# Kernel optimization log

Hardware: AMD Instinct MI355X
Metric: run time of the kernel (lower is better)

Reference implementation:

```python
import jax, jax.numpy as jnp
import numpy as np

N = 100000       # nodes
E = 1600000      # edges (before self loops)
D = 128          # emb_dim
L = 5            # num_layer
NBOND = 62       # num_bond_type
NNODE = 2159     # num_node_type + 2
BN_EPS = 1e-5


def setup_inputs() -> dict:
    key = jax.random.key(0)
    ks = jax.random.split(key, 8)
    x = jax.random.randint(ks[0], (N, 1), 0, NNODE)
    edge_index = jax.random.randint(ks[1], (2, E), 0, N)
    edge_attr = jax.random.randint(ks[2], (E, 1), 0, NBOND)
    x_emb = jax.random.normal(ks[3], (NNODE, D), dtype=jnp.float32) * 0.02
    lin_w = jax.random.normal(ks[4], (L, D, D), dtype=jnp.float32) * (1.0 / np.sqrt(D))
    lin_b = jnp.zeros((L, D), jnp.float32)
    edge_tab = jax.random.normal(ks[5], (L, NBOND, D), dtype=jnp.float32) * 0.02
    bn_gamma = jnp.ones((L, D), jnp.float32)
    bn_beta = jnp.zeros((L, D), jnp.float32)
    return {"x": x, "edge_index": edge_index, "edge_attr": edge_attr,
            "x_emb": x_emb, "lin_w": lin_w, "lin_b": lin_b,
            "edge_tab": edge_tab, "bn_gamma": bn_gamma, "bn_beta": bn_beta}


def reference(x, edge_index, edge_attr, x_emb, lin_w, lin_b, edge_tab, bn_gamma, bn_beta):
    # node embedding lookup: x_embedding(x[:, 0])
    h = x_emb[x[:, 0]]                                  # [N, D]

    # add self loops (same for every layer in the torch code)
    loop = jnp.arange(N)
    src = jnp.concatenate([edge_index[0], loop])        # [E+N] = j (source)
    dst = jnp.concatenate([edge_index[1], loop])        # [E+N] = i (target)
    eids = jnp.concatenate([edge_attr[:, 0], jnp.zeros((N,), edge_attr.dtype)])

    # GCN symmetric norm: deg from row (=src), deg_inv_sqrt[row]*deg_inv_sqrt[col]
    deg = jax.ops.segment_sum(jnp.ones(src.shape, h.dtype), src, num_segments=N)
    dinv = jnp.where(deg > 0, jax.lax.rsqrt(deg), jnp.zeros_like(deg))
    norm = (dinv[src] * dinv[dst])[:, None]             # [E+N, 1]

    for l in range(L):
        # linear transform of nodes
        hl = h @ lin_w[l].T + lin_b[l]                  # [N, D]
        # message: norm * (x_j + edge_embedding), gather from source nodes
        msg = norm * (hl[src] + edge_tab[l][eids])      # [E+N, D]
        # aggr='add': scatter_add into target nodes
        agg = jax.ops.segment_sum(msg, dst, num_segments=N)  # [N, D]
        # BatchNorm1d (training-mode batch statistics, biased variance)
        mean = agg.mean(axis=0)
        var = jnp.mean((agg - mean) ** 2, axis=0)
        h = (agg - mean) * jax.lax.rsqrt(var + BN_EPS) * bn_gamma[l] + bn_beta[l]
        if l < L - 1:
            h = jax.nn.relu(h)
        # dropout with drop_ratio=0 is identity
    # JK == 'last'
    return h
```

## Files before the change

kernel.cpp:

```cpp
#include <hip/hip_runtime.h>

#define NN 100000
#define NE 1600000
#define NT (NE + NN)
#define DD 128
#define NL 5
#define NB 62
#define BN_EPS 1e-5f
#define NBUCK 391
#define PSUMNB 6250
#define RED1 128

typedef unsigned short ushort_t;
typedef unsigned int uint_t;
typedef short bf8 __attribute__((ext_vector_type(8)));
typedef float f32x4 __attribute__((ext_vector_type(4)));

static __device__ __forceinline__ float4 ld4(const float* p) { return *(const float4*)p; }

static __device__ __forceinline__ float bfhi(uint_t u) {
    uint_t x = u & 0xFFFF0000u;
    return __builtin_bit_cast(float, x);
}
static __device__ __forceinline__ float bflo(uint_t u) {
    uint_t x = u << 16;
    return __builtin_bit_cast(float, x);
}
static __device__ __forceinline__ ushort_t f2bf(float f) {
    uint_t u = __builtin_bit_cast(uint_t, f);
    u += 0x7FFFu + ((u >> 16) & 1u);
    return (ushort_t)(u >> 16);
}

static __device__ __forceinline__ void accum8(float* acc, uint4 hv, uint4 ev, float nr) {
    acc[0] = fmaf(nr, bflo(hv.x) + bflo(ev.x), acc[0]);
    acc[1] = fmaf(nr, bfhi(hv.x) + bfhi(ev.x), acc[1]);
    acc[2] = fmaf(nr, bflo(hv.y) + bflo(ev.y), acc[2]);
    acc[3] = fmaf(nr, bfhi(hv.y) + bfhi(ev.y), acc[3]);
    acc[4] = fmaf(nr, bflo(hv.z) + bflo(ev.z), acc[4]);
    acc[5] = fmaf(nr, bfhi(hv.z) + bfhi(ev.z), acc[5]);
    acc[6] = fmaf(nr, bflo(hv.w) + bflo(ev.w), acc[6]);
    acc[7] = fmaf(nr, bfhi(hv.w) + bfhi(ev.w), acc[7]);
}


__global__ void k_init(int* gbh_d, int* gbh_s, float* scale, float* shift,
                       int* row_ptr) {
    int i = blockIdx.x * 256 + threadIdx.x;
    if (i < NBUCK) { gbh_d[i] = 0; gbh_s[i] = 0; }
    if (i < DD) { scale[i] = 1.f; shift[i] = 0.f; }
    if (i == 0) row_ptr[NN] = NT;
}

__global__ void k_cvt(const float* __restrict__ src, ushort_t* __restrict__ dst,
                      int total) {
    int i = blockIdx.x * 256 + threadIdx.x;
    if (i < total) dst[i] = f2bf(src[i]);
}

__global__ __launch_bounds__(256) void k_binhist(const int* __restrict__ ei,
                                                 int* __restrict__ gbh_d,
                                                 int* __restrict__ gbh_s) {
    __shared__ int hd[NBUCK], hs[NBUCK];
    int tid = threadIdx.x;
    for (int b = tid; b < NBUCK; b += 256) { hd[b] = 0; hs[b] = 0; }
    __syncthreads();
    for (int idx = blockIdx.x * 256 + tid; idx < NT; idx += gridDim.x * 256) {
        int d = (idx < NE) ? ei[NE + idx] : idx - NE;
        atomicAdd(&hd[d >> 8], 1);
        if (idx < NE) atomicAdd(&hs[ei[idx] >> 8], 1);
    }
    __syncthreads();
    for (int b = tid; b < NBUCK; b += 256) {
        if (hd[b]) atomicAdd(&gbh_d[b], hd[b]);
        if (hs[b]) atomicAdd(&gbh_s[b], hs[b]);
    }
}

__global__ void k_scan391(const int* __restrict__ gbh_d, const int* __restrict__ gbh_s,
                          int* __restrict__ bb_d, int* __restrict__ cur_d,
                          int* __restrict__ bb_s, int* __restrict__ cur_s) {
    __shared__ int s[512];
    const int* g = blockIdx.x ? gbh_s : gbh_d;
    int* bb = blockIdx.x ? bb_s : bb_d;
    int* cur = blockIdx.x ? cur_s : cur_d;
    int t = threadIdx.x;
    int v = (t < NBUCK) ? g[t] : 0;
    s[t] = v;
    __syncthreads();
    for (int off = 1; off < 512; off <<= 1) {
        int val = (t >= off) ? s[t - off] : 0;
        __syncthreads();
        s[t] += val;
        __syncthreads();
    }
    if (t < NBUCK) { int e = s[t] - v; bb[t] = e; cur[t] = e; }
    if (t == 511) bb[NBUCK] = s[511];
}

#define CHUNK 4096
__global__ __launch_bounds__(256) void k_scat2(const int* __restrict__ ei,
                                               const int* __restrict__ ea,
                                               int* __restrict__ cur_d,
                                               int* __restrict__ cur_s,
                                               uint_t* __restrict__ rec_d,
                                               int* __restrict__ rec_s) {
    __shared__ int lhd[NBUCK], lbd[NBUCK], lhs[NBUCK], lbs[NBUCK];
    int tid = threadIdx.x;
    for (int b = tid; b < NBUCK; b += 256) { lhd[b] = 0; lhs[b] = 0; }
    __syncthreads();
    int base = blockIdx.x * CHUNK;
    uint_t rd[16];
    int rs[16], bkd[16], bks[16];
#pragma unroll
    for (int k = 0; k < 16; ++k) {
        int idx = base + tid + k * 256;
        bkd[k] = -1; bks[k] = -1;
        if (idx < NT) {
            int s, d, eid;
            if (idx < NE) {
                s = ei[idx]; d = ei[NE + idx]; eid = ea[idx];
                bks[k] = s >> 8; rs[k] = s;
                atomicAdd(&lhs[bks[k]], 1);
            } else {
                s = d = idx - NE; eid = 0;
            }
            bkd[k] = d >> 8;
            rd[k] = (uint_t)s | ((uint_t)eid << 17) | ((uint_t)(d & 255) << 24);
            atomicAdd(&lhd[bkd[k]], 1);
        }
    }
    __syncthreads();
    for (int b = tid; b < NBUCK; b += 256) {
        if (lhd[b]) lbd[b] = atomicAdd(&cur_d[b], lhd[b]);
        if (lhs[b]) lbs[b] = atomicAdd(&cur_s[b], lhs[b]);
    }
    __syncthreads();
    for (int b = tid; b < NBUCK; b += 256) { lhd[b] = 0; lhs[b] = 0; }
    __syncthreads();
#pragma unroll
    for (int k = 0; k < 16; ++k) {
        if (bkd[k] >= 0) {
            int rk = atomicAdd(&lhd[bkd[k]], 1);
            rec_d[lbd[bkd[k]] + rk] = rd[k];
        }
        if (bks[k] >= 0) {
            int rk = atomicAdd(&lhs[bks[k]], 1);
            rec_s[lbs[bks[k]] + rk] = rs[k];
        }
    }
}

__global__ __launch_bounds__(256) void k_srcfin(const int* __restrict__ rec,
                                                const int* __restrict__ bb,
                                                float* __restrict__ dinv) {
    __shared__ int h[256];
    int tid = threadIdx.x;
    h[tid] = 0;
    __syncthreads();
    int lo = bb[blockIdx.x], hi = bb[blockIdx.x + 1];
    for (int i = lo + tid; i < hi; i += 256) atomicAdd(&h[rec[i] & 255], 1);
    __syncthreads();
    int v = blockIdx.x * 256 + tid;
    if (v < NN) dinv[v] = rsqrtf((float)(h[tid] + 1));
}

__global__ __launch_bounds__(256) void k_dstfin(const uint_t* __restrict__ rec,
                                                const int* __restrict__ bb,
                                                const float* __restrict__ dinv,
                                                int* __restrict__ row_ptr,
                                                int* __restrict__ s_pack,
                                                float* __restrict__ s_norm) {
    __shared__ int h[256], sc[256], rpE[256];
    int tid = threadIdx.x;
    h[tid] = 0;
    __syncthreads();
    int lo = bb[blockIdx.x], hi = bb[blockIdx.x + 1];
    for (int i = lo + tid; i < hi; i += 256) atomicAdd(&h[(rec[i] >> 24) & 255], 1);
    __syncthreads();
    sc[tid] = h[tid];
    __syncthreads();
    for (int off = 1; off < 256; off <<= 1) {
        int val = (tid >= off) ? sc[tid - off] : 0;
        __syncthreads();
        sc[tid] += val;
        __syncthreads();
    }
    rpE[tid] = sc[tid] - h[tid];
    int v = blockIdx.x * 256 + tid;
    if (v < NN) row_ptr[v] = lo + rpE[tid];
    h[tid] = 0;
    __syncthreads();
    for (int i = lo + tid; i < hi; i += 256) {
        uint_t u = rec[i];
        int dl = (u >> 24) & 255;
        int rk = atomicAdd(&h[dl], 1);
        int slot = lo + rpE[dl] + rk;
        int s = u & 0x1FFFF;
        int e = (u >> 17) & 0x3F;
        s_pack[slot] = s | (e << 20);
        s_norm[slot] = dinv[s] * dinv[(blockIdx.x << 8) + dl];
    }
}

__global__ void k_h0b(const int* __restrict__ x, const float* __restrict__ emb,
                      ushort_t* __restrict__ Xb, int n) {
    int v = blockIdx.x * 16 + (threadIdx.x >> 4);
    if (v >= n) return;
    int c8 = (threadIdx.x & 15) * 8;
    const float* src = &emb[x[v] * DD + c8];
    uint_t pk[4];
#pragma unroll
    for (int j = 0; j < 4; ++j)
        pk[j] = (uint_t)f2bf(src[2 * j]) | ((uint_t)f2bf(src[2 * j + 1]) << 16);
    *(uint4*)&Xb[(size_t)v * DD + c8] = make_uint4(pk[0], pk[1], pk[2], pk[3]);
}


__global__ __launch_bounds__(256, 2) void k_gemm(const ushort_t* __restrict__ Xb,
                                                 const ushort_t* __restrict__ Wb,
                                                 const float* __restrict__ bias,
                                                 const float* __restrict__ scale,
                                                 const float* __restrict__ shift,
                                                 ushort_t* __restrict__ C,
                                                 int n, int relu) {
    __shared__ ushort_t As[128 * DD];
    __shared__ ushort_t Bs[128 * DD];
    const int tid = threadIdx.x;
    const int r0 = blockIdx.x * 128;
    const int rl = tid >> 4;
    const int kg = tid & 15;

    float sc[8], sh[8];
    *(float4*)&sc[0] = ld4(&scale[kg * 8]);
    *(float4*)&sc[4] = ld4(&scale[kg * 8 + 4]);
    *(float4*)&sh[0] = ld4(&shift[kg * 8]);
    *(float4*)&sh[4] = ld4(&shift[kg * 8 + 4]);

#pragma unroll
    for (int it = 0; it < 8; ++it) {
        int row = rl + it * 16;
        int grow = r0 + row;
        uint4 v = make_uint4(0, 0, 0, 0);
        if (grow < n) v = *(const uint4*)&Xb[(size_t)grow * DD + kg * 8];
        uint_t pk[4];
        const uint_t* pv = (const uint_t*)&v;
#pragma unroll
        for (int j = 0; j < 4; ++j) {
            float lo = fmaf(bflo(pv[j]), sc[2 * j], sh[2 * j]);
            float hi = fmaf(bfhi(pv[j]), sc[2 * j + 1], sh[2 * j + 1]);
            if (relu) { lo = fmaxf(lo, 0.f); hi = fmaxf(hi, 0.f); }
            pk[j] = (uint_t)f2bf(lo) | ((uint_t)f2bf(hi) << 16);
        }
        *(uint4*)&As[row * DD + (kg ^ (row & 7)) * 8] = make_uint4(pk[0], pk[1], pk[2], pk[3]);
        uint4 wv = *(const uint4*)&Wb[row * DD + kg * 8];
        *(uint4*)&Bs[row * DD + (kg ^ (row & 7)) * 8] = wv;
    }
    __syncthreads();

    const int w = tid >> 6;
    const int lane = tid & 63;
    const int lr = lane & 15;
    const int lg = lane >> 4;

    f32x4 acc[2][8];
#pragma unroll
    for (int rf = 0; rf < 2; ++rf)
#pragma unroll
        for (int cf = 0; cf < 8; ++cf)
#pragma unroll
            for (int r = 0; r < 4; ++r) acc[rf][cf][r] = 0.f;

#pragma unroll
    for (int ks = 0; ks < 4; ++ks) {
        int kgg = ks * 4 + lg;
        bf8 a0, a1;
        {
            int row = w * 32 + lr;
            a0 = *(bf8*)&As[row * DD + (kgg ^ (row & 7)) * 8];
            row += 16;
            a1 = *(bf8*)&As[row * DD + (kgg ^ (row & 7)) * 8];
        }
#pragma unroll
        for (int cf = 0; cf < 8; ++cf) {
            int col = cf * 16 + lr;
            bf8 b = *(bf8*)&Bs[col * DD + (kgg ^ (col & 7)) * 8];
            acc[0][cf] = __builtin_amdgcn_mfma_f32_16x16x32_bf16(a0, b, acc[0][cf], 0, 0, 0);
            acc[1][cf] = __builtin_amdgcn_mfma_f32_16x16x32_bf16(a1, b, acc[1][cf], 0, 0, 0);
        }
    }

#pragma unroll
    for (int cf = 0; cf < 8; ++cf) {
        int col = cf * 16 + lr;
        float bi = bias[col];
#pragma unroll
        for (int rf = 0; rf < 2; ++rf) {
#pragma unroll
            for (int r = 0; r < 4; ++r) {
                int grow = r0 + w * 32 + rf * 16 + lg * 4 + r;
                if (grow < n) C[(size_t)grow * DD + col] = f2bf(acc[rf][cf][r] + bi);
            }
        }
    }
}

__global__ __launch_bounds__(256) void k_agg(const ushort_t* __restrict__ hl,
                                             const ushort_t* __restrict__ etab,
                                             const int* __restrict__ row_ptr,
                                             const int* __restrict__ s_pack,
                                             const float* __restrict__ s_norm,
                                             ushort_t* __restrict__ aggb,
                                             float* __restrict__ psumA,
                                             float* __restrict__ psumB, int n) {
    __shared__ float lsA[4][DD], lsB[4][DD];
    int tid = threadIdx.x;

    int v = blockIdx.x * 16 + (tid >> 4);
    int lane8 = (tid & 15) * 8;
    int p0 = row_ptr[v], p1 = row_ptr[v + 1];
    float acc[8];
#pragma unroll
    for (int j = 0; j < 8; ++j) acc[j] = 0.f;

    int p = p0;
    for (; p + 4 <= p1; p += 4) {
        int c0 = s_pack[p], c1 = s_pack[p + 1], c2 = s_pack[p + 2], c3 = s_pack[p + 3];
        float n0 = s_norm[p], n1 = s_norm[p + 1], n2 = s_norm[p + 2], n3 = s_norm[p + 3];
        uint4 h0 = *(const uint4*)&hl[(size_t)(c0 & 0xFFFFF) * DD + lane8];
        uint4 h1 = *(const uint4*)&hl[(size_t)(c1 & 0xFFFFF) * DD + lane8];
        uint4 h2 = *(const uint4*)&hl[(size_t)(c2 & 0xFFFFF) * DD + lane8];
        uint4 h3 = *(const uint4*)&hl[(size_t)(c3 & 0xFFFFF) * DD + lane8];
        uint4 e0 = *(const uint4*)&etab[(c0 >> 20) * DD + lane8];
        uint4 e1 = *(const uint4*)&etab[(c1 >> 20) * DD + lane8];
        uint4 e2 = *(const uint4*)&etab[(c2 >> 20) * DD + lane8];
        uint4 e3 = *(const uint4*)&etab[(c3 >> 20) * DD + lane8];
        accum8(acc, h0, e0, n0);
        accum8(acc, h1, e1, n1);
        accum8(acc, h2, e2, n2);
        accum8(acc, h3, e3, n3);
    }
    for (; p < p1; ++p) {
        int c = s_pack[p];
        float nr = s_norm[p];
        uint4 hv = *(const uint4*)&hl[(size_t)(c & 0xFFFFF) * DD + lane8];
        uint4 ev = *(const uint4*)&etab[(c >> 20) * DD + lane8];
        accum8(acc, hv, ev, nr);
    }

    uint_t pk[4];
#pragma unroll
    for (int j = 0; j < 4; ++j)
        pk[j] = (uint_t)f2bf(acc[2 * j]) | ((uint_t)f2bf(acc[2 * j + 1]) << 16);
    *(uint4*)&aggb[(size_t)v * DD + lane8] = make_uint4(pk[0], pk[1], pk[2], pk[3]);

    float s0[8], s1[8];
#pragma unroll
    for (int j = 0; j < 8; ++j) { s0[j] = acc[j]; s1[j] = acc[j] * acc[j]; }
#pragma unroll
    for (int m = 16; m <= 32; m <<= 1) {
#pragma unroll
        for (int j = 0; j < 8; ++j) {
            s0[j] += __shfl_xor(s0[j], m);
            s1[j] += __shfl_xor(s1[j], m);
        }
    }
    int wv = tid >> 6;
    int lane = tid & 63;
    if (lane < 16) {
#pragma unroll
        for (int j = 0; j < 8; ++j) {
            lsA[wv][lane8 + j] = s0[j];
            lsB[wv][lane8 + j] = s1[j];
        }
    }
    __syncthreads();
    if (tid < DD) {
        psumA[(size_t)blockIdx.x * DD + tid] =
            lsA[0][tid] + lsA[1][tid] + lsA[2][tid] + lsA[3][tid];
        psumB[(size_t)blockIdx.x * DD + tid] =
            lsB[0][tid] + lsB[1][tid] + lsB[2][tid] + lsB[3][tid];
    }
}

__global__ __launch_bounds__(256) void k_bnred(const float* __restrict__ psumA,
                                               const float* __restrict__ psumB,
                                               float* __restrict__ partA,
                                               float* __restrict__ partB) {
    __shared__ float sa[2][DD], sb[2][DD];
    int d = threadIdx.x & 127;
    int half = threadIdx.x >> 7;
    float a = 0.f, b = 0.f;
    int iend = min(blockIdx.x * 49 + 49, PSUMNB);
    for (int i = blockIdx.x * 49 + half; i < iend; i += 2) {
        a += psumA[(size_t)i * DD + d];
        b += psumB[(size_t)i * DD + d];
    }
    sa[half][d] = a; sb[half][d] = b;
    __syncthreads();
    if (threadIdx.x < DD) {
        partA[blockIdx.x * DD + d] = sa[0][d] + sa[1][d];
        partB[blockIdx.x * DD + d] = sb[0][d] + sb[1][d];
    }
}

__global__ __launch_bounds__(256) void k_bnfin(const float* __restrict__ partA,
                                               const float* __restrict__ partB,
                                               const float* __restrict__ gamma,
                                               const float* __restrict__ beta,
                                               float* __restrict__ scale,
                                               float* __restrict__ shift, int n) {
    __shared__ float sa[2][DD], sb[2][DD];
    int d = threadIdx.x & 127;
    int half = threadIdx.x >> 7;
    float a = 0.f, b = 0.f;
    for (int i = half; i < RED1; i += 2) {
        a += partA[i * DD + d];
        b += partB[i * DD + d];
    }
    sa[half][d] = a; sb[half][d] = b;
    __syncthreads();
    if (threadIdx.x < DD) {
        float s = sa[0][d] + sa[1][d];
        float ss = sb[0][d] + sb[1][d];
        float mean = s / (float)n;
        float var = ss / (float)n - mean * mean;
        float sc = gamma[d] * rsqrtf(var + BN_EPS);
        scale[d] = sc;
        shift[d] = beta[d] - mean * sc;
    }
}

__global__ void k_bnapply(const ushort_t* __restrict__ Xb, float* __restrict__ out,
                          const float* __restrict__ scale,
                          const float* __restrict__ shift, int total8) {
    int i = blockIdx.x * blockDim.x + threadIdx.x;
    int stride = gridDim.x * blockDim.x;
    for (; i < total8; i += stride) {
        int c8 = (i & 15) * 8;
        uint4 v = *(const uint4*)&Xb[(size_t)i * 8];
        float4 sc0 = ld4(&scale[c8]), sc1 = ld4(&scale[c8 + 4]);
        float4 sh0 = ld4(&shift[c8]), sh1 = ld4(&shift[c8 + 4]);
        float4 o0, o1;
        o0.x = fmaf(bflo(v.x), sc0.x, sh0.x);
        o0.y = fmaf(bfhi(v.x), sc0.y, sh0.y);
        o0.z = fmaf(bflo(v.y), sc0.z, sh0.z);
        o0.w = fmaf(bfhi(v.y), sc0.w, sh0.w);
        o1.x = fmaf(bflo(v.z), sc1.x, sh1.x);
        o1.y = fmaf(bfhi(v.z), sc1.y, sh1.y);
        o1.z = fmaf(bflo(v.w), sc1.z, sh1.z);
        o1.w = fmaf(bfhi(v.w), sc1.w, sh1.w);
        *(float4*)&out[(size_t)i * 8] = o0;
        *(float4*)&out[(size_t)i * 8 + 4] = o1;
    }
}


extern "C" void kernel_launch(void* const* d_in, const int* in_sizes, int n_in,
                              void* d_out, int out_size, void* d_ws, size_t ws_size,
                              hipStream_t stream) {
    const int* x        = (const int*)d_in[0];
    const int* ei       = (const int*)d_in[1];
    const int* ea       = (const int*)d_in[2];
    const float* x_emb  = (const float*)d_in[3];
    const float* lin_w  = (const float*)d_in[4];
    const float* lin_b  = (const float*)d_in[5];
    const float* etab   = (const float*)d_in[6];
    const float* gamma  = (const float*)d_in[7];
    const float* beta   = (const float*)d_in[8];
    float* OUT = (float*)d_out;

    char* w = (char*)d_ws;
    size_t off = 0;
    auto alloc = [&](size_t bytes) -> void* {
        off = (off + 255) & ~(size_t)255;
        void* p = w + off;
        off += bytes;
        return p;
    };
    ushort_t* Xb     = (ushort_t*)alloc((size_t)NN * DD * 2);
    ushort_t* hl     = (ushort_t*)alloc((size_t)NN * DD * 2);
    ushort_t* etabb  = (ushort_t*)alloc((size_t)NL * NB * DD * 2);
    ushort_t* Wb     = (ushort_t*)alloc((size_t)NL * DD * DD * 2);
    uint_t* rec_d    = (uint_t*)alloc((size_t)NT * 4);
    int*    rec_s    = (int*)alloc((size_t)NE * 4);
    int*   s_pack    = (int*)alloc((size_t)NT * 4);
    float* s_norm    = (float*)alloc((size_t)NT * 4);
    int*   rowp      = (int*)alloc((size_t)(NN + 1) * 4);
    float* dinv      = (float*)alloc((size_t)NN * 4);
    int*   gbh_d     = (int*)alloc((size_t)NBUCK * 4);
    int*   gbh_s     = (int*)alloc((size_t)NBUCK * 4);
    int*   bb_d      = (int*)alloc((size_t)(NBUCK + 1) * 4);
    int*   bb_s      = (int*)alloc((size_t)(NBUCK + 1) * 4);
    int*   cur_d     = (int*)alloc((size_t)NBUCK * 4);
    int*   cur_s     = (int*)alloc((size_t)NBUCK * 4);
    float* psumA     = (float*)alloc((size_t)DD * PSUMNB * 4);
    float* psumB     = (float*)alloc((size_t)DD * PSUMNB * 4);
    float* partA     = (float*)alloc((size_t)DD * RED1 * 4);
    float* partB     = (float*)alloc((size_t)DD * RED1 * 4);
    float* scale     = (float*)alloc((size_t)DD * 4);
    float* shift     = (float*)alloc((size_t)DD * 4);

    const int etabTot = NL * NB * DD;
    const int wTot = NL * DD * DD;

    k_init<<<(NN + 255) / 256, 256, 0, stream>>>(gbh_d, gbh_s, scale, shift, rowp);
    k_cvt<<<(etabTot + 255) / 256, 256, 0, stream>>>(etab, etabb, etabTot);
    k_cvt<<<(wTot + 255) / 256, 256, 0, stream>>>(lin_w, Wb, wTot);
    k_binhist<<<256, 256, 0, stream>>>(ei, gbh_d, gbh_s);
    k_scan391<<<2, 512, 0, stream>>>(gbh_d, gbh_s, bb_d, cur_d, bb_s, cur_s);
    k_scat2<<<(NT + CHUNK - 1) / CHUNK, 256, 0, stream>>>(ei, ea, cur_d, cur_s,
                                                          rec_d, rec_s);
    k_srcfin<<<NBUCK, 256, 0, stream>>>(rec_s, bb_s, dinv);
    k_dstfin<<<NBUCK, 256, 0, stream>>>(rec_d, bb_d, dinv, rowp, s_pack, s_norm);
    k_h0b<<<(NN + 15) / 16, 256, 0, stream>>>(x, x_emb, Xb, NN);

    for (int l = 0; l < NL; ++l) {
        k_gemm<<<(NN + 127) / 128, 256, 0, stream>>>(Xb, Wb + (size_t)l * DD * DD,
                                                     lin_b + (size_t)l * DD,
                                                     scale, shift, hl, NN, l > 0 ? 1 : 0);
        k_agg<<<PSUMNB, 256, 0, stream>>>(hl, etabb + (size_t)l * NB * DD,
                                          rowp, s_pack, s_norm, Xb, psumA, psumB, NN);
        k_bnred<<<RED1, 256, 0, stream>>>(psumA, psumB, partA, partB);
        k_bnfin<<<1, 256, 0, stream>>>(partA, partB, gamma + (size_t)l * DD,
                                       beta + (size_t)l * DD, scale, shift, NN);
    }
    k_bnapply<<<(NN * DD / 8 + 255) / 256, 256, 0, stream>>>(Xb, OUT, scale, shift,
                                                             NN * DD / 8);
}
```

Before: 733.3 us.

## Split GEMM K into two halves with register prefetch; unroll gather by eight

The GEMM now stages K in two 64-wide halves and uses half the shared memory. The second half's global loads are issued before the first half's MFMAs so their latency overlaps compute, and launch_bounds no longer pins two blocks per CU. The aggregation kernel gains an 8-edge unrolled loop that issues more independent gathers before accumulating, raising memory-level parallelism. The cost is higher register pressure, which may lower occupancy, plus an extra barrier in the GEMM.

```diff
diff --git a/kernel.cpp b/kernel.cpp
--- a/kernel.cpp
+++ b/kernel.cpp
@@ -217,52 +217,66 @@
 }
 
 
-__global__ __launch_bounds__(256, 2) void k_gemm(const ushort_t* __restrict__ Xb,
-                                                 const ushort_t* __restrict__ Wb,
-                                                 const float* __restrict__ bias,
-                                                 const float* __restrict__ scale,
-                                                 const float* __restrict__ shift,
-                                                 ushort_t* __restrict__ C,
-                                                 int n, int relu) {
-    __shared__ ushort_t As[128 * DD];
-    __shared__ ushort_t Bs[128 * DD];
+__global__ __launch_bounds__(256) void k_gemm(const ushort_t* __restrict__ Xb,
+                                              const ushort_t* __restrict__ Wb,
+                                              const float* __restrict__ bias,
+                                              const float* __restrict__ scale,
+                                              const float* __restrict__ shift,
+                                              ushort_t* __restrict__ C,
+                                              int n, int relu) {
+    __shared__ ushort_t As[128 * 64];
+    __shared__ ushort_t Bs[128 * 64];
     const int tid = threadIdx.x;
     const int r0 = blockIdx.x * 128;
-    const int rl = tid >> 4;
-    const int kg = tid & 15;
-
-    float sc[8], sh[8];
-    *(float4*)&sc[0] = ld4(&scale[kg * 8]);
-    *(float4*)&sc[4] = ld4(&scale[kg * 8 + 4]);
-    *(float4*)&sh[0] = ld4(&shift[kg * 8]);
-    *(float4*)&sh[4] = ld4(&shift[kg * 8 + 4]);
-
-#pragma unroll
-    for (int it = 0; it < 8; ++it) {
-        int row = rl + it * 16;
-        int grow = r0 + row;
-        uint4 v = make_uint4(0, 0, 0, 0);
-        if (grow < n) v = *(const uint4*)&Xb[(size_t)grow * DD + kg * 8];
-        uint_t pk[4];
-        const uint_t* pv = (const uint_t*)&v;
-#pragma unroll
-        for (int j = 0; j < 4; ++j) {
-            float lo = fmaf(bflo(pv[j]), sc[2 * j], sh[2 * j]);
-            float hi = fmaf(bfhi(pv[j]), sc[2 * j + 1], sh[2 * j + 1]);
-            if (relu) { lo = fmaxf(lo, 0.f); hi = fmaxf(hi, 0.f); }
-            pk[j] = (uint_t)f2bf(lo) | ((uint_t)f2bf(hi) << 16);
-        }
-        *(uint4*)&As[row * DD + (kg ^ (row & 7)) * 8] = make_uint4(pk[0], pk[1], pk[2], pk[3]);
-        uint4 wv = *(const uint4*)&Wb[row * DD + kg * 8];
-        *(uint4*)&Bs[row * DD + (kg ^ (row & 7)) * 8] = wv;
-    }
-    __syncthreads();
+    const int skg = tid & 7;
+    const int srow = tid >> 3;
 
     const int w = tid >> 6;
     const int lane = tid & 63;
     const int lr = lane & 15;
     const int lg = lane >> 4;
 
+    float sc0[8], sh0[8], sc1[8], sh1[8];
+    *(float4*)&sc0[0] = ld4(&scale[skg * 8]);     *(float4*)&sc0[4] = ld4(&scale[skg * 8 + 4]);
+    *(float4*)&sh0[0] = ld4(&shift[skg * 8]);     *(float4*)&sh0[4] = ld4(&shift[skg * 8 + 4]);
+    *(float4*)&sc1[0] = ld4(&scale[64 + skg * 8]); *(float4*)&sc1[4] = ld4(&scale[64 + skg * 8 + 4]);
+    *(float4*)&sh1[0] = ld4(&shift[64 + skg * 8]); *(float4*)&sh1[4] = ld4(&shift[64 + skg * 8 + 4]);
+
+    uint4 ar[4], br[4];
+#pragma unroll
+    for (int i = 0; i < 4; ++i) {
+        int row = srow + i * 32;
+        int grow = r0 + row;
+        ar[i] = make_uint4(0, 0, 0, 0);
+        if (grow < n) ar[i] = *(const uint4*)&Xb[(size_t)grow * DD + skg * 8];
+        br[i] = *(const uint4*)&Wb[row * DD + skg * 8];
+    }
+#pragma unroll
+    for (int i = 0; i < 4; ++i) {
+        int row = srow + i * 32;
+        uint_t pk[4];
+        const uint_t* pv = (const uint_t*)&ar[i];
+#pragma unroll
+        for (int j = 0; j < 4; ++j) {
+            float lo = fmaf(bflo(pv[j]), sc0[2 * j], sh0[2 * j]);
+            float hi = fmaf(bfhi(pv[j]), sc0[2 * j + 1], sh0[2 * j + 1]);
+            if (relu) { lo = fmaxf(lo, 0.f); hi = fmaxf(hi, 0.f); }
+            pk[j] = (uint_t)f2bf(lo) | ((uint_t)f2bf(hi) << 16);
+        }
+        *(uint4*)&As[row * 64 + (skg ^ (row & 7)) * 8] = make_uint4(pk[0], pk[1], pk[2], pk[3]);
+        *(uint4*)&Bs[row * 64 + (skg ^ (row & 7)) * 8] = br[i];
+    }
+    __syncthreads();
+
+#pragma unroll
+    for (int i = 0; i < 4; ++i) {
+        int row = srow + i * 32;
+        int grow = r0 + row;
+        ar[i] = make_uint4(0, 0, 0, 0);
+        if (grow < n) ar[i] = *(const uint4*)&Xb[(size_t)grow * DD + 64 + skg * 8];
+        br[i] = *(const uint4*)&Wb[row * DD + 64 + skg * 8];
+    }
+
     f32x4 acc[2][8];
 #pragma unroll
     for (int rf = 0; rf < 2; ++rf)
@@ -272,19 +286,56 @@
             for (int r = 0; r < 4; ++r) acc[rf][cf][r] = 0.f;
 
 #pragma unroll
-    for (int ks = 0; ks < 4; ++ks) {
+    for (int ks = 0; ks < 2; ++ks) {
         int kgg = ks * 4 + lg;
         bf8 a0, a1;
         {
             int row = w * 32 + lr;
-            a0 = *(bf8*)&As[row * DD + (kgg ^ (row & 7)) * 8];
+            a0 = *(bf8*)&As[row * 64 + (kgg ^ (row & 7)) * 8];
             row += 16;
-            a1 = *(bf8*)&As[row * DD + (kgg ^ (row & 7)) * 8];
+            a1 = *(bf8*)&As[row * 64 + (kgg ^ (row & 7)) * 8];
         }
 #pragma unroll
         for (int cf = 0; cf < 8; ++cf) {
             int col = cf * 16 + lr;
-            bf8 b = *(bf8*)&Bs[col * DD + (kgg ^ (col & 7)) * 8];
+            bf8 b = *(bf8*)&Bs[col * 64 + (kgg ^ (col & 7)) * 8];
+            acc[0][cf] = __builtin_amdgcn_mfma_f32_16x16x32_bf16(a0, b, acc[0][cf], 0, 0, 0);
+            acc[1][cf] = __builtin_amdgcn_mfma_f32_16x16x32_bf16(a1, b, acc[1][cf], 0, 0, 0);
+        }
+    }
+    __syncthreads();
+
+#pragma unroll
+    for (int i = 0; i < 4; ++i) {
+        int row = srow + i * 32;
+        uint_t pk[4];
+        const uint_t* pv = (const uint_t*)&ar[i];
+#pragma unroll
+        for (int j = 0; j < 4; ++j) {
+            float lo = fmaf(bflo(pv[j]), sc1[2 * j], sh1[2 * j]);
+            float hi = fmaf(bfhi(pv[j]), sc1[2 * j + 1], sh1[2 * j + 1]);
+            if (relu) { lo = fmaxf(lo, 0.f); hi = fmaxf(hi, 0.f); }
+            pk[j] = (uint_t)f2bf(lo) | ((uint_t)f2bf(hi) << 16);
+        }
+        *(uint4*)&As[row * 64 + (skg ^ (row & 7)) * 8] = make_uint4(pk[0], pk[1], pk[2], pk[3]);
+        *(uint4*)&Bs[row * 64 + (skg ^ (row & 7)) * 8] = br[i];
+    }
+    __syncthreads();
+
+#pragma unroll
+    for (int ks = 0; ks < 2; ++ks) {
+        int kgg = ks * 4 + lg;
+        bf8 a0, a1;
+        {
+            int row = w * 32 + lr;
+            a0 = *(bf8*)&As[row * 64 + (kgg ^ (row & 7)) * 8];
+            row += 16;
+            a1 = *(bf8*)&As[row * 64 + (kgg ^ (row & 7)) * 8];
+        }
+#pragma unroll
+        for (int cf = 0; cf < 8; ++cf) {
+            int col = cf * 16 + lr;
+            bf8 b = *(bf8*)&Bs[col * 64 + (kgg ^ (col & 7)) * 8];
             acc[0][cf] = __builtin_amdgcn_mfma_f32_16x16x32_bf16(a0, b, acc[0][cf], 0, 0, 0);
             acc[1][cf] = __builtin_amdgcn_mfma_f32_16x16x32_bf16(a1, b, acc[1][cf], 0, 0, 0);
         }
@@ -324,21 +375,35 @@
     for (int j = 0; j < 8; ++j) acc[j] = 0.f;
 
     int p = p0;
+    for (; p + 8 <= p1; p += 8) {
+        int c[8]; float nr[8]; uint4 h[8], e[8];
+#pragma unroll
+        for (int q = 0; q < 8; ++q) c[q] = s_pack[p + q];
+#pragma unroll
+        for (int q = 0; q < 8; ++q) nr[q] = s_norm[p + q];
+#pragma unroll
+        for (int q = 0; q < 8; ++q)
+            h[q] = *(const uint4*)&hl[(size_t)(c[q] & 0xFFFFF) * DD + lane8];
+#pragma unroll
+        for (int q = 0; q < 8; ++q)
+            e[q] = *(const uint4*)&etab[(c[q] >> 20) * DD + lane8];
+#pragma unroll
+        for (int q = 0; q < 8; ++q) accum8(acc, h[q], e[q], nr[q]);
+    }
     for (; p + 4 <= p1; p += 4) {
-        int c0 = s_pack[p], c1 = s_pack[p + 1], c2 = s_pack[p + 2], c3 = s_pack[p + 3];
-        float n0 = s_norm[p], n1 = s_norm[p + 1], n2 = s_norm[p + 2], n3 = s_norm[p + 3];
-        uint4 h0 = *(const uint4*)&hl[(size_t)(c0 & 0xFFFFF) * DD + lane8];
-        uint4 h1 = *(const uint4*)&hl[(size_t)(c1 & 0xFFFFF) * DD + lane8];
-        uint4 h2 = *(const uint4*)&hl[(size_t)(c2 & 0xFFFFF) * DD + lane8];
-        uint4 h3 = *(const uint4*)&hl[(size_t)(c3 & 0xFFFFF) * DD + lane8];
-        uint4 e0 = *(const uint4*)&etab[(c0 >> 20) * DD + lane8];
-        uint4 e1 = *(const uint4*)&etab[(c1 >> 20) * DD + lane8];
-        uint4 e2 = *(const uint4*)&etab[(c2 >> 20) * DD + lane8];
-        uint4 e3 = *(const uint4*)&etab[(c3 >> 20) * DD + lane8];
-        accum8(acc, h0, e0, n0);
-        accum8(acc, h1, e1, n1);
-        accum8(acc, h2, e2, n2);
-        accum8(acc, h3, e3, n3);
+        int c[4]; float nr[4]; uint4 h[4], e[4];
+#pragma unroll
+        for (int q = 0; q < 4; ++q) c[q] = s_pack[p + q];
+#pragma unroll
+        for (int q = 0; q < 4; ++q) nr[q] = s_norm[p + q];
+#pragma unroll
+        for (int q = 0; q < 4; ++q)
+            h[q] = *(const uint4*)&hl[(size_t)(c[q] & 0xFFFFF) * DD + lane8];
+#pragma unroll
+        for (int q = 0; q < 4; ++q)
+            e[q] = *(const uint4*)&etab[(c[q] >> 20) * DD + lane8];
+#pragma unroll
+        for (int q = 0; q < 4; ++q) accum8(acc, h[q], e[q], nr[q]);
     }
     for (; p < p1; ++p) {
         int c = s_pack[p];
```

Result: slower. 813.3 us (+10.9%).

## Split aggregation into feature slices per block and pack index with norm

Applied to the files above, without the earlier changes.

The aggregation kernel now splits the 128 feature columns into four 32-column slices, each handled by a separate block. Each block covers 64 nodes, with 4 threads per node instead of 16. The aim is a smaller per-block working set of gathered hl columns, so each block's gathers touch a narrower range and may get better L2 locality. The cost is that every edge's index and norm are read four times. The source index and norm are also interleaved into one int2 array so each edge costs a single 8-byte load. The partial-sum layout and the first BN reduction are adjusted to the new chunk count.

```diff
diff --git a/kernel.cpp b/kernel.cpp
--- a/kernel.cpp
+++ b/kernel.cpp
@@ -8,7 +8,7 @@
 #define NB 62
 #define BN_EPS 1e-5f
 #define NBUCK 391
-#define PSUMNB 6250
+#define NCH 1563
 #define RED1 128
 
 typedef unsigned short ushort_t;
@@ -169,8 +169,7 @@
                                                 const int* __restrict__ bb,
                                                 const float* __restrict__ dinv,
                                                 int* __restrict__ row_ptr,
-                                                int* __restrict__ s_pack,
-                                                float* __restrict__ s_norm) {
+                                                int2* __restrict__ s_pn) {
     __shared__ int h[256], sc[256], rpE[256];
     int tid = threadIdx.x;
     h[tid] = 0;
@@ -198,8 +197,8 @@
         int slot = lo + rpE[dl] + rk;
         int s = u & 0x1FFFF;
         int e = (u >> 17) & 0x3F;
-        s_pack[slot] = s | (e << 20);
-        s_norm[slot] = dinv[s] * dinv[(blockIdx.x << 8) + dl];
+        float nm = dinv[s] * dinv[(blockIdx.x << 8) + dl];
+        s_pn[slot] = make_int2(s | (e << 20), __float_as_int(nm));
     }
 }
 
@@ -308,57 +307,59 @@
 __global__ __launch_bounds__(256) void k_agg(const ushort_t* __restrict__ hl,
                                              const ushort_t* __restrict__ etab,
                                              const int* __restrict__ row_ptr,
-                                             const int* __restrict__ s_pack,
-                                             const float* __restrict__ s_norm,
+                                             const int2* __restrict__ s_pn,
                                              ushort_t* __restrict__ aggb,
                                              float* __restrict__ psumA,
                                              float* __restrict__ psumB, int n) {
-    __shared__ float lsA[4][DD], lsB[4][DD];
+    __shared__ float lsA[4][32], lsB[4][32];
     int tid = threadIdx.x;
-
-    int v = blockIdx.x * 16 + (tid >> 4);
-    int lane8 = (tid & 15) * 8;
-    int p0 = row_ptr[v], p1 = row_ptr[v + 1];
+    int slice = blockIdx.x & 3;
+    int chunk = blockIdx.x >> 2;
+    int nl = tid >> 2;
+    int sub = tid & 3;
+    int v = chunk * 64 + nl;
+    int sOff = slice * 32 + sub * 8;
+
     float acc[8];
 #pragma unroll
     for (int j = 0; j < 8; ++j) acc[j] = 0.f;
 
-    int p = p0;
-    for (; p + 4 <= p1; p += 4) {
-        int c0 = s_pack[p], c1 = s_pack[p + 1], c2 = s_pack[p + 2], c3 = s_pack[p + 3];
-        float n0 = s_norm[p], n1 = s_norm[p + 1], n2 = s_norm[p + 2], n3 = s_norm[p + 3];
-        uint4 h0 = *(const uint4*)&hl[(size_t)(c0 & 0xFFFFF) * DD + lane8];
-        uint4 h1 = *(const uint4*)&hl[(size_t)(c1 & 0xFFFFF) * DD + lane8];
-        uint4 h2 = *(const uint4*)&hl[(size_t)(c2 & 0xFFFFF) * DD + lane8];
-        uint4 h3 = *(const uint4*)&hl[(size_t)(c3 & 0xFFFFF) * DD + lane8];
-        uint4 e0 = *(const uint4*)&etab[(c0 >> 20) * DD + lane8];
-        uint4 e1 = *(const uint4*)&etab[(c1 >> 20) * DD + lane8];
-        uint4 e2 = *(const uint4*)&etab[(c2 >> 20) * DD + lane8];
-        uint4 e3 = *(const uint4*)&etab[(c3 >> 20) * DD + lane8];
-        accum8(acc, h0, e0, n0);
-        accum8(acc, h1, e1, n1);
-        accum8(acc, h2, e2, n2);
-        accum8(acc, h3, e3, n3);
-    }
-    for (; p < p1; ++p) {
-        int c = s_pack[p];
-        float nr = s_norm[p];
-        uint4 hv = *(const uint4*)&hl[(size_t)(c & 0xFFFFF) * DD + lane8];
-        uint4 ev = *(const uint4*)&etab[(c >> 20) * DD + lane8];
-        accum8(acc, hv, ev, nr);
-    }
-
-    uint_t pk[4];
-#pragma unroll
-    for (int j = 0; j < 4; ++j)
-        pk[j] = (uint_t)f2bf(acc[2 * j]) | ((uint_t)f2bf(acc[2 * j + 1]) << 16);
-    *(uint4*)&aggb[(size_t)v * DD + lane8] = make_uint4(pk[0], pk[1], pk[2], pk[3]);
+    if (v < n) {
+        int p0 = row_ptr[v], p1 = row_ptr[v + 1];
+        int p = p0;
+        for (; p + 4 <= p1; p += 4) {
+            int2 a0 = s_pn[p], a1 = s_pn[p + 1], a2 = s_pn[p + 2], a3 = s_pn[p + 3];
+            uint4 h0 = *(const uint4*)&hl[(size_t)(a0.x & 0xFFFFF) * DD + sOff];
+            uint4 h1 = *(const uint4*)&hl[(size_t)(a1.x & 0xFFFFF) * DD + sOff];
+            uint4 h2 = *(const uint4*)&hl[(size_t)(a2.x & 0xFFFFF) * DD + sOff];
+            uint4 h3 = *(const uint4*)&hl[(size_t)(a3.x & 0xFFFFF) * DD + sOff];
+            uint4 e0 = *(const uint4*)&etab[(a0.x >> 20) * DD + sOff];
+            uint4 e1 = *(const uint4*)&etab[(a1.x >> 20) * DD + sOff];
+            uint4 e2 = *(const uint4*)&etab[(a2.x >> 20) * DD + sOff];
+            uint4 e3 = *(const uint4*)&etab[(a3.x >> 20) * DD + sOff];
+            accum8(acc, h0, e0, __int_as_float(a0.y));
+            accum8(acc, h1, e1, __int_as_float(a1.y));
+            accum8(acc, h2, e2, __int_as_float(a2.y));
+            accum8(acc, h3, e3, __int_as_float(a3.y));
+        }
+        for (; p < p1; ++p) {
+            int2 a = s_pn[p];
+            uint4 hv = *(const uint4*)&hl[(size_t)(a.x & 0xFFFFF) * DD + sOff];
+            uint4 ev = *(const uint4*)&etab[(a.x >> 20) * DD + sOff];
+            accum8(acc, hv, ev, __int_as_float(a.y));
+        }
+        uint_t pk[4];
+#pragma unroll
+        for (int j = 0; j < 4; ++j)
+            pk[j] = (uint_t)f2bf(acc[2 * j]) | ((uint_t)f2bf(acc[2 * j + 1]) << 16);
+        *(uint4*)&aggb[(size_t)v * DD + sOff] = make_uint4(pk[0], pk[1], pk[2], pk[3]);
+    }
 
     float s0[8], s1[8];
 #pragma unroll
     for (int j = 0; j < 8; ++j) { s0[j] = acc[j]; s1[j] = acc[j] * acc[j]; }
 #pragma unroll
-    for (int m = 16; m <= 32; m <<= 1) {
+    for (int m = 4; m <= 32; m <<= 1) {
 #pragma unroll
         for (int j = 0; j < 8; ++j) {
             s0[j] += __shfl_xor(s0[j], m);
@@ -367,19 +368,19 @@
     }
     int wv = tid >> 6;
     int lane = tid & 63;
-    if (lane < 16) {
+    if (lane < 4) {
 #pragma unroll
         for (int j = 0; j < 8; ++j) {
-            lsA[wv][lane8 + j] = s0[j];
-            lsB[wv][lane8 + j] = s1[j];
-        }
-    }
-    __syncthreads();
-    if (tid < DD) {
-        psumA[(size_t)blockIdx.x * DD + tid] =
-            lsA[0][tid] + lsA[1][tid] + lsA[2][tid] + lsA[3][tid];
-        psumB[(size_t)blockIdx.x * DD + tid] =
-            lsB[0][tid] + lsB[1][tid] + lsB[2][tid] + lsB[3][tid];
+            lsA[wv][lane * 8 + j] = s0[j];
+            lsB[wv][lane * 8 + j] = s1[j];
+        }
+    }
+    __syncthreads();
+    if (tid < 32) {
+        float a = lsA[0][tid] + lsA[1][tid] + lsA[2][tid] + lsA[3][tid];
+        float b = lsB[0][tid] + lsB[1][tid] + lsB[2][tid] + lsB[3][tid];
+        psumA[(size_t)chunk * DD + slice * 32 + tid] = a;
+        psumB[(size_t)chunk * DD + slice * 32 + tid] = b;
     }
 }
 
@@ -391,8 +392,8 @@
     int d = threadIdx.x & 127;
     int half = threadIdx.x >> 7;
     float a = 0.f, b = 0.f;
-    int iend = min(blockIdx.x * 49 + 49, PSUMNB);
-    for (int i = blockIdx.x * 49 + half; i < iend; i += 2) {
+    int iend = min(blockIdx.x * 13 + 13, NCH);
+    for (int i = blockIdx.x * 13 + half; i < iend; i += 2) {
         a += psumA[(size_t)i * DD + d];
         b += psumB[(size_t)i * DD + d];
     }
@@ -484,8 +485,7 @@
     ushort_t* Wb     = (ushort_t*)alloc((size_t)NL * DD * DD * 2);
     uint_t* rec_d    = (uint_t*)alloc((size_t)NT * 4);
     int*    rec_s    = (int*)alloc((size_t)NE * 4);
-    int*   s_pack    = (int*)alloc((size_t)NT * 4);
-    float* s_norm    = (float*)alloc((size_t)NT * 4);
+    int2*  s_pn      = (int2*)alloc((size_t)NT * 8);
     int*   rowp      = (int*)alloc((size_t)(NN + 1) * 4);
     float* dinv      = (float*)alloc((size_t)NN * 4);
     int*   gbh_d     = (int*)alloc((size_t)NBUCK * 4);
@@ -494,8 +494,8 @@
     int*   bb_s      = (int*)alloc((size_t)(NBUCK + 1) * 4);
     int*   cur_d     = (int*)alloc((size_t)NBUCK * 4);
     int*   cur_s     = (int*)alloc((size_t)NBUCK * 4);
-    float* psumA     = (float*)alloc((size_t)DD * PSUMNB * 4);
-    float* psumB     = (float*)alloc((size_t)DD * PSUMNB * 4);
+    float* psumA     = (float*)alloc((size_t)DD * NCH * 4);
+    float* psumB     = (float*)alloc((size_t)DD * NCH * 4);
     float* partA     = (float*)alloc((size_t)DD * RED1 * 4);
     float* partB     = (float*)alloc((size_t)DD * RED1 * 4);
     float* scale     = (float*)alloc((size_t)DD * 4);
@@ -512,15 +512,15 @@
     k_scat2<<<(NT + CHUNK - 1) / CHUNK, 256, 0, stream>>>(ei, ea, cur_d, cur_s,
                                                           rec_d, rec_s);
     k_srcfin<<<NBUCK, 256, 0, stream>>>(rec_s, bb_s, dinv);
-    k_dstfin<<<NBUCK, 256, 0, stream>>>(rec_d, bb_d, dinv, rowp, s_pack, s_norm);
+    k_dstfin<<<NBUCK, 256, 0, stream>>>(rec_d, bb_d, dinv, rowp, s_pn);
     k_h0b<<<(NN + 15) / 16, 256, 0, stream>>>(x, x_emb, Xb, NN);
 
     for (int l = 0; l < NL; ++l) {
         k_gemm<<<(NN + 127) / 128, 256, 0, stream>>>(Xb, Wb + (size_t)l * DD * DD,
                                                      lin_b + (size_t)l * DD,
                                                      scale, shift, hl, NN, l > 0 ? 1 : 0);
-        k_agg<<<PSUMNB, 256, 0, stream>>>(hl, etabb + (size_t)l * NB * DD,
-                                          rowp, s_pack, s_norm, Xb, psumA, psumB, NN);
+        k_agg<<<4 * NCH, 256, 0, stream>>>(hl, etabb + (size_t)l * NB * DD,
+                                           rowp, s_pn, Xb, psumA, psumB, NN);
         k_bnred<<<RED1, 256, 0, stream>>>(psumA, psumB, partA, partB);
         k_bnfin<<<1, 256, 0, stream>>>(partA, partB, gamma + (size_t)l * DD,
                                        beta + (size_t)l * DD, scale, shift, NN);
```

New measurement: 964.5 us. +31.5%, slower.

## Interleave CSR index/norm arrays and drop LDS staging in GEMM

Applied to the files above, without the earlier changes.

Merges the per-edge packed source/edge-type array and the norm array into a single int2 array, so each aggregation step issues one 8-byte load instead of two separate loads from two streams. The GEMM kernel no longer stages A and W tiles through shared memory. Each wave now loads its A fragments straight from global memory, applies BN+ReLU in registers, and reads W fragments directly from global/L2. Launch bounds are raised to 3 blocks per SM. Without LDS the GEMM relies on cache for W reuse and does uncoalesced-ish fragment loads, which could hurt if L1/L2 hit rates are poor.

```diff
diff --git a/kernel.cpp b/kernel.cpp
--- a/kernel.cpp
+++ b/kernel.cpp
@@ -169,8 +169,7 @@
                                                 const int* __restrict__ bb,
                                                 const float* __restrict__ dinv,
                                                 int* __restrict__ row_ptr,
-                                                int* __restrict__ s_pack,
-                                                float* __restrict__ s_norm) {
+                                                int2* __restrict__ s_pn) {
     __shared__ int h[256], sc[256], rpE[256];
     int tid = threadIdx.x;
     h[tid] = 0;
@@ -198,8 +197,8 @@
         int slot = lo + rpE[dl] + rk;
         int s = u & 0x1FFFF;
         int e = (u >> 17) & 0x3F;
-        s_pack[slot] = s | (e << 20);
-        s_norm[slot] = dinv[s] * dinv[(blockIdx.x << 8) + dl];
+        float nm = dinv[s] * dinv[(blockIdx.x << 8) + dl];
+        s_pn[slot] = make_int2(s | (e << 20), __float_as_int(nm));
     }
 }
 
@@ -217,47 +216,35 @@
 }
 
 
-__global__ __launch_bounds__(256, 2) void k_gemm(const ushort_t* __restrict__ Xb,
+static __device__ __forceinline__ bf8 bn8(uint4 v, float4 sc0, float4 sc1,
+                                          float4 sh0, float4 sh1, int relu) {
+    const uint_t* pv = (const uint_t*)&v;
+    float f[8];
+    f[0] = fmaf(bflo(pv[0]), sc0.x, sh0.x); f[1] = fmaf(bfhi(pv[0]), sc0.y, sh0.y);
+    f[2] = fmaf(bflo(pv[1]), sc0.z, sh0.z); f[3] = fmaf(bfhi(pv[1]), sc0.w, sh0.w);
+    f[4] = fmaf(bflo(pv[2]), sc1.x, sh1.x); f[5] = fmaf(bfhi(pv[2]), sc1.y, sh1.y);
+    f[6] = fmaf(bflo(pv[3]), sc1.z, sh1.z); f[7] = fmaf(bfhi(pv[3]), sc1.w, sh1.w);
+    if (relu) {
+#pragma unroll
+        for (int j = 0; j < 8; ++j) f[j] = fmaxf(f[j], 0.f);
+    }
+    uint_t pk[4];
+#pragma unroll
+    for (int j = 0; j < 4; ++j)
+        pk[j] = (uint_t)f2bf(f[2 * j]) | ((uint_t)f2bf(f[2 * j + 1]) << 16);
+    uint4 r = make_uint4(pk[0], pk[1], pk[2], pk[3]);
+    return __builtin_bit_cast(bf8, r);
+}
+
+__global__ __launch_bounds__(256, 3) void k_gemm(const ushort_t* __restrict__ Xb,
                                                  const ushort_t* __restrict__ Wb,
                                                  const float* __restrict__ bias,
                                                  const float* __restrict__ scale,
                                                  const float* __restrict__ shift,
                                                  ushort_t* __restrict__ C,
                                                  int n, int relu) {
-    __shared__ ushort_t As[128 * DD];
-    __shared__ ushort_t Bs[128 * DD];
     const int tid = threadIdx.x;
     const int r0 = blockIdx.x * 128;
-    const int rl = tid >> 4;
-    const int kg = tid & 15;
-
-    float sc[8], sh[8];
-    *(float4*)&sc[0] = ld4(&scale[kg * 8]);
-    *(float4*)&sc[4] = ld4(&scale[kg * 8 + 4]);
-    *(float4*)&sh[0] = ld4(&shift[kg * 8]);
-    *(float4*)&sh[4] = ld4(&shift[kg * 8 + 4]);
-
-#pragma unroll
-    for (int it = 0; it < 8; ++it) {
-        int row = rl + it * 16;
-        int grow = r0 + row;
-        uint4 v = make_uint4(0, 0, 0, 0);
-        if (grow < n) v = *(const uint4*)&Xb[(size_t)grow * DD + kg * 8];
-        uint_t pk[4];
-        const uint_t* pv = (const uint_t*)&v;
-#pragma unroll
-        for (int j = 0; j < 4; ++j) {
-            float lo = fmaf(bflo(pv[j]), sc[2 * j], sh[2 * j]);
-            float hi = fmaf(bfhi(pv[j]), sc[2 * j + 1], sh[2 * j + 1]);
-            if (relu) { lo = fmaxf(lo, 0.f); hi = fmaxf(hi, 0.f); }
-            pk[j] = (uint_t)f2bf(lo) | ((uint_t)f2bf(hi) << 16);
-        }
-        *(uint4*)&As[row * DD + (kg ^ (row & 7)) * 8] = make_uint4(pk[0], pk[1], pk[2], pk[3]);
-        uint4 wv = *(const uint4*)&Wb[row * DD + kg * 8];
-        *(uint4*)&Bs[row * DD + (kg ^ (row & 7)) * 8] = wv;
-    }
-    __syncthreads();
-
     const int w = tid >> 6;
     const int lane = tid & 63;
     const int lr = lane & 15;
@@ -273,18 +260,22 @@
 
 #pragma unroll
     for (int ks = 0; ks < 4; ++ks) {
-        int kgg = ks * 4 + lg;
-        bf8 a0, a1;
-        {
-            int row = w * 32 + lr;
-            a0 = *(bf8*)&As[row * DD + (kgg ^ (row & 7)) * 8];
-            row += 16;
-            a1 = *(bf8*)&As[row * DD + (kgg ^ (row & 7)) * 8];
-        }
+        const int kb = (ks * 4 + lg) * 8;
+        float4 sc0 = ld4(&scale[kb]), sc1 = ld4(&scale[kb + 4]);
+        float4 sh0 = ld4(&shift[kb]), sh1 = ld4(&shift[kb + 4]);
+
+        int row0 = r0 + w * 32 + lr;
+        int row1 = row0 + 16;
+        uint4 va = make_uint4(0, 0, 0, 0), vb = make_uint4(0, 0, 0, 0);
+        if (row0 < n) va = *(const uint4*)&Xb[(size_t)row0 * DD + kb];
+        if (row1 < n) vb = *(const uint4*)&Xb[(size_t)row1 * DD + kb];
+        bf8 a0 = bn8(va, sc0, sc1, sh0, sh1, relu);
+        bf8 a1 = bn8(vb, sc0, sc1, sh0, sh1, relu);
+
 #pragma unroll
         for (int cf = 0; cf < 8; ++cf) {
             int col = cf * 16 + lr;
-            bf8 b = *(bf8*)&Bs[col * DD + (kgg ^ (col & 7)) * 8];
+            bf8 b = *(const bf8*)&Wb[(size_t)col * DD + kb];
             acc[0][cf] = __builtin_amdgcn_mfma_f32_16x16x32_bf16(a0, b, acc[0][cf], 0, 0, 0);
             acc[1][cf] = __builtin_amdgcn_mfma_f32_16x16x32_bf16(a1, b, acc[1][cf], 0, 0, 0);
         }
@@ -308,8 +299,7 @@
 __global__ __launch_bounds__(256) void k_agg(const ushort_t* __restrict__ hl,
                                              const ushort_t* __restrict__ etab,
                                              const int* __restrict__ row_ptr,
-                                             const int* __restrict__ s_pack,
-                                             const float* __restrict__ s_norm,
+                                             const int2* __restrict__ s_pn,
                                              ushort_t* __restrict__ aggb,
                                              float* __restrict__ psumA,
                                              float* __restrict__ psumB, int n) {
@@ -325,27 +315,25 @@
 
     int p = p0;
     for (; p + 4 <= p1; p += 4) {
-        int c0 = s_pack[p], c1 = s_pack[p + 1], c2 = s_pack[p + 2], c3 = s_pack[p + 3];
-        float n0 = s_norm[p], n1 = s_norm[p + 1], n2 = s_norm[p + 2], n3 = s_norm[p + 3];
-        uint4 h0 = *(const uint4*)&hl[(size_t)(c0 & 0xFFFFF) * DD + lane8];
-        uint4 h1 = *(const uint4*)&hl[(size_t)(c1 & 0xFFFFF) * DD + lane8];
-        uint4 h2 = *(const uint4*)&hl[(size_t)(c2 & 0xFFFFF) * DD + lane8];
-        uint4 h3 = *(const uint4*)&hl[(size_t)(c3 & 0xFFFFF) * DD + lane8];
-        uint4 e0 = *(const uint4*)&etab[(c0 >> 20) * DD + lane8];
-        uint4 e1 = *(const uint4*)&etab[(c1 >> 20) * DD + lane8];
-        uint4 e2 = *(const uint4*)&etab[(c2 >> 20) * DD + lane8];
-        uint4 e3 = *(const uint4*)&etab[(c3 >> 20) * DD + lane8];
-        accum8(acc, h0, e0, n0);
-        accum8(acc, h1, e1, n1);
-        accum8(acc, h2, e2, n2);
-        accum8(acc, h3, e3, n3);
+        int2 a0 = s_pn[p], a1 = s_pn[p + 1], a2 = s_pn[p + 2], a3 = s_pn[p + 3];
+        uint4 h0 = *(const uint4*)&hl[(size_t)(a0.x & 0xFFFFF) * DD + lane8];
+        uint4 h1 = *(const uint4*)&hl[(size_t)(a1.x & 0xFFFFF) * DD + lane8];
+        uint4 h2 = *(const uint4*)&hl[(size_t)(a2.x & 0xFFFFF) * DD + lane8];
+        uint4 h3 = *(const uint4*)&hl[(size_t)(a3.x & 0xFFFFF) * DD + lane8];
+        uint4 e0 = *(const uint4*)&etab[(a0.x >> 20) * DD + lane8];
+        uint4 e1 = *(const uint4*)&etab[(a1.x >> 20) * DD + lane8];
+        uint4 e2 = *(const uint4*)&etab[(a2.x >> 20) * DD + lane8];
+        uint4 e3 = *(const uint4*)&etab[(a3.x >> 20) * DD + lane8];
+        accum8(acc, h0, e0, __int_as_float(a0.y));
+        accum8(acc, h1, e1, __int_as_float(a1.y));
+        accum8(acc, h2, e2, __int_as_float(a2.y));
+        accum8(acc, h3, e3, __int_as_float(a3.y));
     }
     for (; p < p1; ++p) {
-        int c = s_pack[p];
-        float nr = s_norm[p];
-        uint4 hv = *(const uint4*)&hl[(size_t)(c & 0xFFFFF) * DD + lane8];
-        uint4 ev = *(const uint4*)&etab[(c >> 20) * DD + lane8];
-        accum8(acc, hv, ev, nr);
+        int2 a = s_pn[p];
+        uint4 hv = *(const uint4*)&hl[(size_t)(a.x & 0xFFFFF) * DD + lane8];
+        uint4 ev = *(const uint4*)&etab[(a.x >> 20) * DD + lane8];
+        accum8(acc, hv, ev, __int_as_float(a.y));
     }
 
     uint_t pk[4];
@@ -484,8 +472,7 @@
     ushort_t* Wb     = (ushort_t*)alloc((size_t)NL * DD * DD * 2);
     uint_t* rec_d    = (uint_t*)alloc((size_t)NT * 4);
     int*    rec_s    = (int*)alloc((size_t)NE * 4);
-    int*   s_pack    = (int*)alloc((size_t)NT * 4);
-    float* s_norm    = (float*)alloc((size_t)NT * 4);
+    int2*  s_pn      = (int2*)alloc((size_t)NT * 8);
     int*   rowp      = (int*)alloc((size_t)(NN + 1) * 4);
     float* dinv      = (float*)alloc((size_t)NN * 4);
     int*   gbh_d     = (int*)alloc((size_t)NBUCK * 4);
@@ -512,7 +499,7 @@
     k_scat2<<<(NT + CHUNK - 1) / CHUNK, 256, 0, stream>>>(ei, ea, cur_d, cur_s,
                                                           rec_d, rec_s);
     k_srcfin<<<NBUCK, 256, 0, stream>>>(rec_s, bb_s, dinv);
-    k_dstfin<<<NBUCK, 256, 0, stream>>>(rec_d, bb_d, dinv, rowp, s_pack, s_norm);
+    k_dstfin<<<NBUCK, 256, 0, stream>>>(rec_d, bb_d, dinv, rowp, s_pn);
     k_h0b<<<(NN + 15) / 16, 256, 0, stream>>>(x, x_emb, Xb, NN);
 
     for (int l = 0; l < NL; ++l) {
@@ -520,7 +507,7 @@
                                                      lin_b + (size_t)l * DD,
                                                      scale, shift, hl, NN, l > 0 ? 1 : 0);
         k_agg<<<PSUMNB, 256, 0, stream>>>(hl, etabb + (size_t)l * NB * DD,
-                                          rowp, s_pack, s_norm, Xb, psumA, psumB, NN);
+                                          rowp, s_pn, Xb, psumA, psumB, NN);
         k_bnred<<<RED1, 256, 0, stream>>>(psumA, psumB, partA, partB);
         k_bnfin<<<1, 256, 0, stream>>>(partA, partB, gamma + (size_t)l * DD,
                                        beta + (size_t)l * DD, scale, shift, NN);
```

Result: slower. 755.2 us (+3.0%).
